# Kernel optimization log

Measured on AMD Instinct MI355X. Metric: run time of the kernel, lower is better.

## Reference

```python
import jax, jax.numpy as jnp
import numpy as np

D_MODEL = 1024
NHEAD = 16
D_HEAD = D_MODEL // NHEAD


def setup_inputs() -> dict:
    key = jax.random.key(0)
    ks = jax.random.split(key, 5)
    s_in = 1.0 / np.sqrt(D_MODEL)
    x = jax.random.normal(ks[0], (2, 2048, D_MODEL), dtype=jnp.float32)
    Wqkv = jax.random.uniform(ks[1], (D_MODEL, 3 * D_MODEL), jnp.float32, -s_in, s_in)
    bqkv = jax.random.uniform(ks[2], (3 * D_MODEL,), jnp.float32, -s_in, s_in)
    Wproj = jax.random.uniform(ks[3], (D_MODEL, D_MODEL), jnp.float32, -s_in, s_in)
    bproj = jax.random.uniform(ks[4], (D_MODEL,), jnp.float32, -s_in, s_in)
    return {"x": x, "Wqkv": Wqkv, "bqkv": bqkv, "Wproj": Wproj, "bproj": bproj}


def reference(x, Wqkv, bqkv, Wproj, bproj):
    B, N, D = x.shape
    qkv = x @ Wqkv + bqkv                       # [B, N, 3D]
    q, k, v = jnp.split(qkv, 3, axis=-1)
    # [B, N, D] -> [B, H, N, d]
    def to_heads(t):
        return t.reshape(B, N, NHEAD, D_HEAD).transpose(0, 2, 1, 3)
    q, k, v = to_heads(q), to_heads(k), to_heads(v)
    scale = 1.0 / np.sqrt(D_HEAD).astype(np.float32)
    attn = jnp.einsum('bhqd,bhkd->bhqk', q, k) * scale
    attn = jax.nn.softmax(attn, axis=-1)
    y = jnp.einsum('bhqk,bhkd->bhqd', attn, v)  # [B, H, N, d]
    y = y.transpose(0, 2, 1, 3).reshape(B, N, D)
    return y @ Wproj + bproj
```

## Files before the change

kernel.cpp:

```cpp
#include <hip/hip_runtime.h>
#include <hip/hip_bf16.h>
#include <stdint.h>

typedef __hip_bfloat16 bf16;
typedef __attribute__((ext_vector_type(8))) short short8;
typedef __attribute__((ext_vector_type(4))) short short4v;
typedef __attribute__((ext_vector_type(4))) float f32x4;

#define L2E 1.44269504088896f

__device__ __forceinline__ void gload_lds16(const bf16* g, bf16* l) {
#if __has_builtin(__builtin_amdgcn_global_load_lds)
  __builtin_amdgcn_global_load_lds(
      (const __attribute__((address_space(1))) void*)(uintptr_t)g,
      (__attribute__((address_space(3))) void*)(uint32_t)(uintptr_t)l,
      16, 0, 0);
#else
  int lane = threadIdx.x & 63;
  *(short8*)(l + lane * 8) = *(const short8*)(g + lane * 8);
#endif
}

__global__ __launch_bounds__(256) void convert_k(const float* __restrict__ in,
                                                 bf16* __restrict__ out, int n) {
  int i = (blockIdx.x * 256 + threadIdx.x) * 8;
  if (i >= n) return;
  f32x4 v0 = *(const f32x4*)(in + i);
  f32x4 v1 = *(const f32x4*)(in + i + 4);
  short8 r;
  bf16* rb = (bf16*)&r;
#pragma unroll
  for (int j = 0; j < 4; ++j) {
    rb[j] = __float2bfloat16(v0[j]);
    rb[4 + j] = __float2bfloat16(v1[j]);
  }
  *(short8*)(out + i) = r;
}

__global__ __launch_bounds__(256) void transpose_k(const float* __restrict__ in,
                                                   bf16* __restrict__ out,
                                                   int R, int C) {
  __shared__ __align__(16) bf16 t[64][72];
  const int r0 = blockIdx.y * 64, c0 = blockIdx.x * 64;
  const int rr = threadIdx.x >> 3, cc = (threadIdx.x & 7) * 8;
#pragma unroll
  for (int rep = 0; rep < 2; ++rep) {
    int y = rr + rep * 32;
    const float* p = in + (size_t)(r0 + y) * C + c0 + cc;
    f32x4 v0 = *(const f32x4*)p;
    f32x4 v1 = *(const f32x4*)(p + 4);
#pragma unroll
    for (int j = 0; j < 4; ++j) {
      t[cc + j][y] = __float2bfloat16(v0[j]);
      t[cc + 4 + j][y] = __float2bfloat16(v1[j]);
    }
  }
  __syncthreads();
#pragma unroll
  for (int rep = 0; rep < 2; ++rep) {
    int y = rr + rep * 32;
    short8 v = *(const short8*)&t[y][cc];
    *(short8*)(out + (size_t)(c0 + y) * R + r0 + cc) = v;
  }
}

template <int MODE, int TM>
__global__ __launch_bounds__(256, 2)
void gemm_bt(const bf16* __restrict__ A, const bf16* __restrict__ Bt,
             const float* __restrict__ bias, float* __restrict__ outp,
             bf16* __restrict__ Qd, bf16* __restrict__ Kd, bf16* __restrict__ Vt,
             int M, int Nn, int K) {
  constexpr int MI = TM / 32;
  __shared__ __align__(16) bf16 As[TM * 32];
  __shared__ __align__(16) bf16 Bs[128 * 32];

  const int tid = threadIdx.x;
  const int wave = tid >> 6, lane = tid & 63;
  const int quad = lane >> 4, l16 = lane & 15;
  const int mw = (wave >> 1) * (TM / 2), nw = (wave & 1) * 64;
  const int m_blk = blockIdx.y * TM, n_blk = blockIdx.x * 128;

  f32x4 acc[MI][4];
#pragma unroll
  for (int i = 0; i < MI; ++i)
#pragma unroll
    for (int j = 0; j < 4; ++j) acc[i][j] = (f32x4){0.f, 0.f, 0.f, 0.f};

  const int rowA = lane >> 2, colA = (lane & 3) * 8;
  const int chunkB = wave * 2;
  const bf16* gB = Bt + (size_t)(n_blk + chunkB * 16 + rowA) * K + colA;
  bf16* lB0 = &Bs[chunkB * 16 * 32];
  bf16* lB1 = &Bs[(chunkB + 1) * 16 * 32];

  const int chunkA = (TM == 128) ? wave * 2 : wave;
  const bf16* gA = A + (size_t)(m_blk + chunkA * 16 + rowA) * K + colA;
  bf16* lA0 = &As[chunkA * 16 * 32];
  bf16* lA1 = &As[(chunkA + 1) * 16 * 32];

  for (int kt = 0; kt < K; kt += 32) {
    gload_lds16(gA, lA0);
    if (TM == 128) gload_lds16(gA + 16 * K, lA1);
    gload_lds16(gB, lB0);
    gload_lds16(gB + 16 * K, lB1);
    gA += 32; gB += 32;
    __syncthreads();
    short8 af[MI], bfv[4];
#pragma unroll
    for (int i = 0; i < MI; ++i)
      af[i] = *(const short8*)&As[(mw + i * 16 + l16) * 32 + quad * 8];
#pragma unroll
    for (int j = 0; j < 4; ++j)
      bfv[j] = *(const short8*)&Bs[(nw + j * 16 + l16) * 32 + quad * 8];
#pragma unroll
    for (int i = 0; i < MI; ++i)
#pragma unroll
      for (int j = 0; j < 4; ++j)
        acc[i][j] = __builtin_amdgcn_mfma_f32_16x16x32_bf16(af[i], bfv[j],
                                                            acc[i][j], 0, 0, 0);
    __syncthreads();
  }

#pragma unroll
  for (int j = 0; j < 4; ++j) {
    const int ncol = n_blk + nw + j * 16 + l16;
    const float bval = bias[ncol];
#pragma unroll
    for (int i = 0; i < MI; ++i) {
      const int mrow0 = m_blk + mw + i * 16 + quad * 4;
#pragma unroll
      for (int r = 0; r < 4; ++r) {
        const float val = acc[i][j][r] + bval;
        const int mrow = mrow0 + r;
        if (MODE == 0) {
          const int part = ncol >> 10;
          const int rem = ncol & 1023;
          const int h = rem >> 6, dh = rem & 63;
          const int b = mrow >> 11, t = mrow & 2047;
          const size_t bh = (size_t)(b * 16 + h);
          if (part == 0)
            Qd[(bh * 2048 + t) * 64 + dh] = __float2bfloat16(val);
          else if (part == 1)
            Kd[(bh * 2048 + t) * 64 + dh] = __float2bfloat16(val);
          else
            Vt[(bh * 64 + dh) * 2048 + t] = __float2bfloat16(val);
        } else {
          outp[(size_t)mrow * Nn + ncol] = val;
        }
      }
    }
  }
}

__global__ __launch_bounds__(256, 4)
void attn_kernel(const bf16* __restrict__ Qg, const bf16* __restrict__ Kg,
                 const bf16* __restrict__ Vt, bf16* __restrict__ yg) {
  __shared__ __align__(16) bf16 Ks[64][72];
  __shared__ __align__(16) bf16 Vts[64 * 72];
  __shared__ __align__(16) bf16 Ps[64][72];

  const int tid = threadIdx.x;
  const int wave = tid >> 6, lane = tid & 63;
  const int quad = lane >> 4, l16 = lane & 15;
  const int m0 = wave * 16;

  const int bx = blockIdx.x;
  const int qt = bx & 31;
  const int bh = bx >> 5;

  const bf16* Qb = Qg + ((size_t)bh * 2048 + qt * 64) * 64;
  const bf16* Kb = Kg + (size_t)bh * 2048 * 64;
  const bf16* Vtb = Vt + (size_t)bh * 64 * 2048;

  short8 qf[2];
#pragma unroll
  for (int kb = 0; kb < 2; ++kb)
    qf[kb] = *(const short8*)(Qb + (size_t)(m0 + l16) * 64 + kb * 32 + quad * 8);

  f32x4 yacc[4];
#pragma unroll
  for (int nb = 0; nb < 4; ++nb) yacc[nb] = (f32x4){0.f, 0.f, 0.f, 0.f};

  float sum_l = 0.f;
  const float c1 = 0.125f * L2E;

  const int kr = tid >> 3, kc = (tid & 7) * 8;
  const int vdd = tid & 63, vo = tid >> 6;
  const int voff0 = vdd * 72 + (((vo) + (vdd >> 3)) & 7) * 8;
  const int voff1 = vdd * 72 + (((vo + 4) + (vdd >> 3)) & 7) * 8;

  const bf16* Kp0 = Kb + (size_t)kr * 64 + kc;
  const bf16* Kp1 = Kb + (size_t)(kr + 32) * 64 + kc;
  const bf16* Vp0 = Vtb + (size_t)vdd * 2048 + vo * 8;
  const bf16* Vp1 = Vtb + (size_t)vdd * 2048 + (vo + 4) * 8;

  short8 gk0 = *(const short8*)Kp0;
  short8 gk1 = *(const short8*)Kp1;
  short8 gv0 = *(const short8*)Vp0;
  short8 gv1 = *(const short8*)Vp1;

  for (int kt = 0; kt < 2048; kt += 64) {
    *(short8*)&Ks[kr][kc] = gk0;
    *(short8*)&Ks[kr + 32][kc] = gk1;
    *(short8*)&Vts[voff0] = gv0;
    *(short8*)&Vts[voff1] = gv1;
    __syncthreads();

    if (kt + 64 < 2048) {
      gk0 = *(const short8*)(Kp0 + (size_t)(kt + 64) * 64);
      gk1 = *(const short8*)(Kp1 + (size_t)(kt + 64) * 64);
      gv0 = *(const short8*)(Vp0 + kt + 64);
      gv1 = *(const short8*)(Vp1 + kt + 64);
    }

    f32x4 st[4];
#pragma unroll
    for (int i = 0; i < 4; ++i) {
      short8 kf0 = *(const short8*)&Ks[i * 16 + l16][quad * 8];
      short8 kf1 = *(const short8*)&Ks[i * 16 + l16][32 + quad * 8];
      f32x4 a = (f32x4){0.f, 0.f, 0.f, 0.f};
      a = __builtin_amdgcn_mfma_f32_16x16x32_bf16(kf0, qf[0], a, 0, 0, 0);
      a = __builtin_amdgcn_mfma_f32_16x16x32_bf16(kf1, qf[1], a, 0, 0, 0);
      st[i] = a;
    }

    float ssum = 0.f;
#pragma unroll
    for (int i = 0; i < 4; ++i) {
      float p0 = exp2f(st[i][0] * c1);
      float p1 = exp2f(st[i][1] * c1);
      float p2 = exp2f(st[i][2] * c1);
      float p3 = exp2f(st[i][3] * c1);
      ssum += (p0 + p1) + (p2 + p3);
      short4v pk;
      bf16* pkb = (bf16*)&pk;
      pkb[0] = __float2bfloat16(p0);
      pkb[1] = __float2bfloat16(p1);
      pkb[2] = __float2bfloat16(p2);
      pkb[3] = __float2bfloat16(p3);
      *(short4v*)&Ps[m0 + l16][i * 16 + quad * 4] = pk;
    }
    sum_l += ssum;
    asm volatile("s_waitcnt lgkmcnt(0)" ::: "memory");

#pragma unroll
    for (int kb = 0; kb < 2; ++kb) {
      short8 pa = *(const short8*)&Ps[m0 + l16][kb * 32 + quad * 8];
#pragma unroll
      for (int nb = 0; nb < 4; ++nb) {
        const int d = nb * 16 + l16;
        short8 vbf = *(const short8*)&Vts[d * 72 +
            (((kb * 4 + quad) + (d >> 3)) & 7) * 8];
        yacc[nb] =
            __builtin_amdgcn_mfma_f32_16x16x32_bf16(pa, vbf, yacc[nb], 0, 0, 0);
      }
    }
    __syncthreads();
  }

  sum_l += __shfl_xor(sum_l, 16);
  sum_l += __shfl_xor(sum_l, 32);

  const int b = bh >> 4, h = bh & 15;
  const size_t rowbase = (size_t)b * 2048 + qt * 64;
#pragma unroll
  for (int r = 0; r < 4; ++r) {
    const float lv = __shfl(sum_l, quad * 4 + r, 16);
    const float inv = 1.f / lv;
    const int rr = m0 + quad * 4 + r;
#pragma unroll
    for (int nb = 0; nb < 4; ++nb)
      yg[(rowbase + rr) * 1024 + h * 64 + nb * 16 + l16] =
          __float2bfloat16(yacc[nb][r] * inv);
  }
}

extern "C" void kernel_launch(void* const* d_in, const int* in_sizes, int n_in,
                              void* d_out, int out_size, void* d_ws, size_t ws_size,
                              hipStream_t stream) {
  const float* x = (const float*)d_in[0];
  const float* Wqkv = (const float*)d_in[1];
  const float* bqkv = (const float*)d_in[2];
  const float* Wproj = (const float*)d_in[3];
  const float* bproj = (const float*)d_in[4];
  float* out = (float*)d_out;

  if (ws_size < (size_t)40 * 1024 * 1024) return;

  char* ws = (char*)d_ws;
  bf16* xb    = (bf16*)(ws + 0);
  bf16* yd    = (bf16*)(ws + 0);
  bf16* WtQkv = (bf16*)(ws + 8388608);
  bf16* WtP   = (bf16*)(ws + 14680064);
  bf16* Qd    = (bf16*)(ws + 16777216);
  bf16* Kd    = (bf16*)(ws + 25165824);
  bf16* Vten  = (bf16*)(ws + 33554432);

  convert_k<<<2048, 256, 0, stream>>>(x, xb, 4096 * 1024);
  transpose_k<<<dim3(48, 16), 256, 0, stream>>>(Wqkv, WtQkv, 1024, 3072);
  transpose_k<<<dim3(16, 16), 256, 0, stream>>>(Wproj, WtP, 1024, 1024);
  gemm_bt<0, 128><<<dim3(24, 32), 256, 0, stream>>>(
      xb, WtQkv, bqkv, nullptr, Qd, Kd, Vten, 4096, 3072, 1024);
  attn_kernel<<<dim3(1024), 256, 0, stream>>>(Qd, Kd, Vten, yd);
  gemm_bt<1, 64><<<dim3(8, 64), 256, 0, stream>>>(
      yd, WtP, bproj, out, nullptr, nullptr, nullptr, 4096, 1024, 1024);
}
```

Baseline: 213.4 us.

## Merge prep kernels, fold softmax scale into Q, use fast exp2 and packed bf16 stores

Merges the x conversion and both weight transposes into one launch, which removes two kernel launches. The attention scale and the log2(e) factor are folded into Q in the QKV GEMM epilogue, so the softmax loop no longer multiplies each score. That loop now uses the hardware exp2 builtin and packed bf16 conversion. The V-transpose epilogue writes 4 packed bf16 values per store instead of scalar stores. The raw exp2 builtin and pre-scaling Q before bf16 rounding change precision slightly.

```diff
diff --git a/kernel.cpp b/kernel.cpp
--- a/kernel.cpp
+++ b/kernel.cpp
@@ -4,10 +4,31 @@
 
 typedef __hip_bfloat16 bf16;
 typedef __attribute__((ext_vector_type(8))) short short8;
-typedef __attribute__((ext_vector_type(4))) short short4v;
 typedef __attribute__((ext_vector_type(4))) float f32x4;
 
-#define L2E 1.44269504088896f
+#define QSCALE 0.18033688011f
+
+__device__ __forceinline__ float fast_exp2(float x) {
+#if __has_builtin(__builtin_amdgcn_exp2f)
+  return __builtin_amdgcn_exp2f(x);
+#else
+  return exp2f(x);
+#endif
+}
+
+__device__ __forceinline__ uint32_t pack2_bf16(float a, float b) {
+#if __has_builtin(__builtin_amdgcn_cvt_pk_bf16_f32)
+  typedef __attribute__((ext_vector_type(2))) __bf16 bf16x2;
+  bf16x2 v = __builtin_amdgcn_cvt_pk_bf16_f32(a, b);
+  return __builtin_bit_cast(uint32_t, v);
+#else
+  uint32_t ua = __builtin_bit_cast(uint32_t, a);
+  uint32_t ub = __builtin_bit_cast(uint32_t, b);
+  ua += 0x7FFF + ((ua >> 16) & 1);
+  ub += 0x7FFF + ((ub >> 16) & 1);
+  return (ua >> 16) | (ub & 0xFFFF0000u);
+#endif
+}
 
 __device__ __forceinline__ void gload_lds16(const bf16* g, bf16* l) {
 #if __has_builtin(__builtin_amdgcn_global_load_lds)
@@ -21,27 +42,11 @@
 #endif
 }
 
-__global__ __launch_bounds__(256) void convert_k(const float* __restrict__ in,
-                                                 bf16* __restrict__ out, int n) {
-  int i = (blockIdx.x * 256 + threadIdx.x) * 8;
-  if (i >= n) return;
-  f32x4 v0 = *(const f32x4*)(in + i);
-  f32x4 v1 = *(const f32x4*)(in + i + 4);
-  short8 r;
-  bf16* rb = (bf16*)&r;
-#pragma unroll
-  for (int j = 0; j < 4; ++j) {
-    rb[j] = __float2bfloat16(v0[j]);
-    rb[4 + j] = __float2bfloat16(v1[j]);
-  }
-  *(short8*)(out + i) = r;
-}
-
-__global__ __launch_bounds__(256) void transpose_k(const float* __restrict__ in,
-                                                   bf16* __restrict__ out,
-                                                   int R, int C) {
-  __shared__ __align__(16) bf16 t[64][72];
-  const int r0 = blockIdx.y * 64, c0 = blockIdx.x * 64;
+__device__ __forceinline__ void transpose_tile(const float* __restrict__ in,
+                                               bf16* __restrict__ out,
+                                               int R, int C, int bx, int by,
+                                               bf16 (*t)[72]) {
+  const int r0 = by * 64, c0 = bx * 64;
   const int rr = threadIdx.x >> 3, cc = (threadIdx.x & 7) * 8;
 #pragma unroll
   for (int rep = 0; rep < 2; ++rep) {
@@ -61,6 +66,33 @@
     int y = rr + rep * 32;
     short8 v = *(const short8*)&t[y][cc];
     *(short8*)(out + (size_t)(c0 + y) * R + r0 + cc) = v;
+  }
+}
+
+__global__ __launch_bounds__(256)
+void prep_k(const float* __restrict__ x, bf16* __restrict__ xb,
+            const float* __restrict__ Wqkv, bf16* __restrict__ WtQkv,
+            const float* __restrict__ Wproj, bf16* __restrict__ WtP) {
+  __shared__ __align__(16) bf16 t[64][72];
+  const int bid = blockIdx.x;
+  if (bid < 2048) {
+    int i = (bid * 256 + threadIdx.x) * 8;
+    f32x4 v0 = *(const f32x4*)(x + i);
+    f32x4 v1 = *(const f32x4*)(x + i + 4);
+    short8 r;
+    bf16* rb = (bf16*)&r;
+#pragma unroll
+    for (int j = 0; j < 4; ++j) {
+      rb[j] = __float2bfloat16(v0[j]);
+      rb[4 + j] = __float2bfloat16(v1[j]);
+    }
+    *(short8*)(xb + i) = r;
+  } else if (bid < 2048 + 768) {
+    int b = bid - 2048;
+    transpose_tile(Wqkv, WtQkv, 1024, 3072, b % 48, b / 48, t);
+  } else {
+    int b = bid - 2816;
+    transpose_tile(Wproj, WtP, 1024, 1024, b % 16, b / 16, t);
   }
 }
 
@@ -124,28 +156,36 @@
   for (int j = 0; j < 4; ++j) {
     const int ncol = n_blk + nw + j * 16 + l16;
     const float bval = bias[ncol];
-#pragma unroll
-    for (int i = 0; i < MI; ++i) {
-      const int mrow0 = m_blk + mw + i * 16 + quad * 4;
-#pragma unroll
-      for (int r = 0; r < 4; ++r) {
-        const float val = acc[i][j][r] + bval;
-        const int mrow = mrow0 + r;
-        if (MODE == 0) {
-          const int part = ncol >> 10;
-          const int rem = ncol & 1023;
-          const int h = rem >> 6, dh = rem & 63;
-          const int b = mrow >> 11, t = mrow & 2047;
-          const size_t bh = (size_t)(b * 16 + h);
-          if (part == 0)
-            Qd[(bh * 2048 + t) * 64 + dh] = __float2bfloat16(val);
-          else if (part == 1)
-            Kd[(bh * 2048 + t) * 64 + dh] = __float2bfloat16(val);
-          else
-            Vt[(bh * 64 + dh) * 2048 + t] = __float2bfloat16(val);
+    if (MODE == 0) {
+      const int part = ncol >> 10;
+      const int rem = ncol & 1023;
+      const int h = rem >> 6, dh = rem & 63;
+#pragma unroll
+      for (int i = 0; i < MI; ++i) {
+        const int t0 = m_blk + mw + i * 16 + quad * 4;
+        const int b = t0 >> 11, tt = t0 & 2047;
+        const size_t bh = (size_t)(b * 16 + h);
+        if (part == 2) {
+          uint32_t w0 = pack2_bf16(acc[i][j][0] + bval, acc[i][j][1] + bval);
+          uint32_t w1 = pack2_bf16(acc[i][j][2] + bval, acc[i][j][3] + bval);
+          uint2 pk; pk.x = w0; pk.y = w1;
+          *(uint2*)&Vt[(bh * 64 + dh) * 2048 + tt] = pk;
         } else {
-          outp[(size_t)mrow * Nn + ncol] = val;
+          bf16* dst = (part == 0) ? Qd : Kd;
+          const float sc = (part == 0) ? QSCALE : 1.0f;
+#pragma unroll
+          for (int r = 0; r < 4; ++r)
+            dst[(bh * 2048 + tt + r) * 64 + dh] =
+                __float2bfloat16((acc[i][j][r] + bval) * sc);
         }
+      }
+    } else {
+#pragma unroll
+      for (int i = 0; i < MI; ++i) {
+        const int mrow0 = m_blk + mw + i * 16 + quad * 4;
+#pragma unroll
+        for (int r = 0; r < 4; ++r)
+          outp[(size_t)(mrow0 + r) * Nn + ncol] = acc[i][j][r] + bval;
       }
     }
   }
@@ -181,7 +221,6 @@
   for (int nb = 0; nb < 4; ++nb) yacc[nb] = (f32x4){0.f, 0.f, 0.f, 0.f};
 
   float sum_l = 0.f;
-  const float c1 = 0.125f * L2E;
 
   const int kr = tid >> 3, kc = (tid & 7) * 8;
   const int vdd = tid & 63, vo = tid >> 6;
@@ -226,18 +265,15 @@
     float ssum = 0.f;
 #pragma unroll
     for (int i = 0; i < 4; ++i) {
-      float p0 = exp2f(st[i][0] * c1);
-      float p1 = exp2f(st[i][1] * c1);
-      float p2 = exp2f(st[i][2] * c1);
-      float p3 = exp2f(st[i][3] * c1);
+      float p0 = fast_exp2(st[i][0]);
+      float p1 = fast_exp2(st[i][1]);
+      float p2 = fast_exp2(st[i][2]);
+      float p3 = fast_exp2(st[i][3]);
       ssum += (p0 + p1) + (p2 + p3);
-      short4v pk;
-      bf16* pkb = (bf16*)&pk;
-      pkb[0] = __float2bfloat16(p0);
-      pkb[1] = __float2bfloat16(p1);
-      pkb[2] = __float2bfloat16(p2);
-      pkb[3] = __float2bfloat16(p3);
-      *(short4v*)&Ps[m0 + l16][i * 16 + quad * 4] = pk;
+      uint2 pk;
+      pk.x = pack2_bf16(p0, p1);
+      pk.y = pack2_bf16(p2, p3);
+      *(uint2*)&Ps[m0 + l16][i * 16 + quad * 4] = pk;
     }
     sum_l += ssum;
     asm volatile("s_waitcnt lgkmcnt(0)" ::: "memory");
@@ -295,9 +331,7 @@
   bf16* Kd    = (bf16*)(ws + 25165824);
   bf16* Vten  = (bf16*)(ws + 33554432);
 
-  convert_k<<<2048, 256, 0, stream>>>(x, xb, 4096 * 1024);
-  transpose_k<<<dim3(48, 16), 256, 0, stream>>>(Wqkv, WtQkv, 1024, 3072);
-  transpose_k<<<dim3(16, 16), 256, 0, stream>>>(Wproj, WtP, 1024, 1024);
+  prep_k<<<3072, 256, 0, stream>>>(x, xb, Wqkv, WtQkv, Wproj, WtP);
   gemm_bt<0, 128><<<dim3(24, 32), 256, 0, stream>>>(
       xb, WtQkv, bqkv, nullptr, Qd, Kd, Vten, 4096, 3072, 1024);
   attn_kernel<<<dim3(1024), 256, 0, stream>>>(Qd, Kd, Vten, yd);
```

Result: faster. 199.0 us (-6.8%).
